# Kernel optimization log

Measured on AMD Instinct MI355X. Metric: run time of the kernel, lower is better.

## Reference

```python
import jax, jax.numpy as jnp
import numpy as np

BATCH_SIZE = 1024
L2_EPS = 1e-12  # tf.nn.l2_normalize epsilon


def setup_inputs() -> dict:
    key = jax.random.key(0)
    k1, k2, k3 = jax.random.split(key, 3)
    worlds = jax.random.normal(k1, (2048, 64), dtype=jnp.float32)   # (n_worlds, d_worlds)
    W = jax.random.normal(k2, (512, 64, 64), dtype=jnp.float32)     # (n_symbols, d, d)
    nullary = jax.random.randint(k3, (1024, 2), 0, 512, dtype=jnp.int32)  # (N, [batch_idx, symbol_idx])
    return {"worlds": worlds, "W": W, "nullary": nullary}


def reference(worlds, W, nullary):
    # Gather per-symbol weight matrices: (N, d, d)
    W_xs = W[nullary[:, 1]]
    # tensordot(W_xs, worlds, axes=[[2],[1]]) -> (N, d, n_worlds)
    x_s = jnp.einsum('nde,we->ndw', W_xs, worlds)
    # L2 normalize over axis=1 (d), matching tf.nn.l2_normalize semantics
    sq = jnp.sum(jnp.square(x_s), axis=1, keepdims=True)
    x_s = x_s * jax.lax.rsqrt(jnp.maximum(sq, L2_EPS))
    # scatter_nd: additive scatter into (batch_size, d, n_worlds)
    d, n_worlds = worlds.shape[1], worlds.shape[0]
    out = jnp.zeros((BATCH_SIZE, d, n_worlds), dtype=x_s.dtype)
    out = out.at[nullary[:, 0]].add(x_s)
    return out
```

## Files before the change

### kernel.cpp

```cpp
#include <hip/hip_runtime.h>

#define NB      1024
#define NWORLD  2048
#define DDIM    64
#define NWMAT   512
#define CONV_BLOCKS 1088
#define LIST_BLOCKS 128
#define GRID_MAIN   6144
#define STASH_ROW   512
#define STASH_ROWS  9
#define FILL_ROW0   (STASH_ROW + STASH_ROWS)
#define FILL_CHUNKS ((NB - FILL_ROW0) * 16)

#define STASH_BYTE  268435456ull
#define OFF_WBF     0ull
#define OFF_WORLDS  4194304ull
#define OFF_DESC    4456448ull

typedef __attribute__((ext_vector_type(4))) float f32x4;
typedef __attribute__((ext_vector_type(8))) short bf16x8;

__device__ __forceinline__ unsigned short f2bf(float f) {
    union { float f; unsigned u; } v; v.f = f;
    unsigned u = v.u;
    u += 0x7fffu + ((u >> 16) & 1u);
    return (unsigned short)(u >> 16);
}

__global__ __launch_bounds__(256)
void prep(const float* __restrict__ W, const float* __restrict__ worlds,
          const int* __restrict__ nullary, char* outb)
{
    unsigned short* Wbf      = (unsigned short*)(outb + STASH_BYTE + OFF_WBF);
    unsigned short* worldsbf = (unsigned short*)(outb + STASH_BYTE + OFF_WORLDS);
    int* descI               = (int*)(outb + STASH_BYTE + OFF_DESC);

    const int bid = blockIdx.x;
    if (bid < CONV_BLOCKS) {
        const int NWE = NWMAT * DDIM * DDIM;
        int i = (bid * 256 + threadIdx.x) * 8;
        const float* src; unsigned short* dst; int off;
        if (i < NWE) { src = W;      dst = Wbf;      off = i; }
        else         { src = worlds; dst = worldsbf; off = i - NWE; }
        f32x4 a = *reinterpret_cast<const f32x4*>(src + off);
        f32x4 b = *reinterpret_cast<const f32x4*>(src + off + 4);
        bf16x8 r;
        r[0] = (short)f2bf(a[0]); r[1] = (short)f2bf(a[1]);
        r[2] = (short)f2bf(a[2]); r[3] = (short)f2bf(a[3]);
        r[4] = (short)f2bf(b[0]); r[5] = (short)f2bf(b[1]);
        r[6] = (short)f2bf(b[2]); r[7] = (short)f2bf(b[3]);
        *reinterpret_cast<bf16x8*>(dst + off) = r;
        return;
    }
    const int r    = (bid - CONV_BLOCKS) * 4 + (threadIdx.x >> 6);
    const int lane = threadIdx.x & 63;
    int base = 0;
    for (int c = 0; c < NB / 64; ++c) {
        const int n = c * 64 + lane;
        const bool m = (nullary[2 * n] == r);
        const unsigned long long mask = __ballot(m);
        if (m) {
            const int pos = base + __popcll(mask & ((1ull << lane) - 1ull));
            if (pos < 31) descI[r * 32 + 1 + pos] = nullary[2 * n + 1];
        }
        base += __popcll(mask);
    }
    if (lane == 0) descI[r * 32] = (base > 31 ? 31 : base);
}

__global__ __launch_bounds__(256)
void main2(char* outb)
{
    const unsigned short* Wbf      = (const unsigned short*)(outb + STASH_BYTE + OFF_WBF);
    const unsigned short* worldsbf = (const unsigned short*)(outb + STASH_BYTE + OFF_WORLDS);
    const int4* desc4              = (const int4*)(outb + STASH_BYTE + OFF_DESC);
    const int*  descI              = (const int*)desc4;
    float* out                     = (float*)outb;

    const int bid = blockIdx.x;
    const int tid = threadIdx.x;
    const f32x4 z = {0.f, 0.f, 0.f, 0.f};

    if (bid % 3 == 2) {
        const int fid = bid / 3;
        for (int chunk = fid; chunk < FILL_CHUNKS; chunk += 2048) {
            const int r = FILL_ROW0 + (chunk >> 4);
            f32x4* o = reinterpret_cast<f32x4*>(out + (size_t)r * DDIM * NWORLD
                                                + (size_t)(chunk & 15) * 8192) + tid;
            #pragma unroll
            for (int j = 0; j < 8; ++j)
                o[j * 256] = z;
        }
        return;
    }

    const int slot = (bid / 3) * 2 + (bid % 3);
    const int r    = slot >> 3;
    const int wtA  = (slot & 7) * 2;

    const int wave = tid >> 6, lane = tid & 63;
    const int col  = lane & 15, krow = lane >> 4;
    const int drow = tid >> 5;
    const int wl   = (tid & 31) * 4;

    bf16x8 bfrag[2][2][2];
    #pragma unroll
    for (int t = 0; t < 2; ++t)
        #pragma unroll
        for (int sub = 0; sub < 2; ++sub) {
            const int w0 = (wtA + t) * 128 + wave * 32 + sub * 16 + col;
            const unsigned short* wp = worldsbf + (size_t)w0 * DDIM + krow * 8;
            bfrag[t][sub][0] = *reinterpret_cast<const bf16x8*>(wp);
            bfrag[t][sub][1] = *reinterpret_cast<const bf16x8*>(wp + 32);
        }

    const int4 h = desc4[r * 8];
    const int cnt = h.x;
    float* orow = out + (size_t)r * DDIM * NWORLD;

    if (cnt == 0) {
        float* obase = orow + wtA * 128;
        #pragma unroll
        for (int k = 0; k < 16; ++k) {
            const int idx = k * 256 + tid;
            const int d  = idx >> 6;
            const int c4 = (idx & 63) * 4;
            *reinterpret_cast<f32x4*>(obase + (size_t)d * NWORLD + c4) = z;
        }
        return;
    }

    __shared__ float T[DDIM][132];

    f32x4 acc[2][2][4];
    #pragma unroll
    for (int t = 0; t < 2; ++t)
        #pragma unroll
        for (int q = 0; q < 2; ++q)
            #pragma unroll
            for (int m = 0; m < 4; ++m)
                acc[t][q][m] = z;

    for (int mi = 0; mi < cnt; ++mi) {
        int b;
        if      (mi == 0) b = h.y;
        else if (mi == 1) b = h.z;
        else if (mi == 2) b = h.w;
        else              b = descI[r * 32 + 1 + mi];
        const unsigned short* Wb = Wbf + (size_t)b * DDIM * DDIM;
        bf16x8 afrag[4][2];
        #pragma unroll
        for (int mt = 0; mt < 4; ++mt) {
            const unsigned short* ap = Wb + (size_t)(mt * 16 + col) * DDIM + krow * 8;
            afrag[mt][0] = *reinterpret_cast<const bf16x8*>(ap);
            afrag[mt][1] = *reinterpret_cast<const bf16x8*>(ap + 32);
        }
        #pragma unroll
        for (int t = 0; t < 2; ++t)
            #pragma unroll
            for (int sub = 0; sub < 2; ++sub) {
                f32x4 x[4];
                #pragma unroll
                for (int mt = 0; mt < 4; ++mt) {
                    f32x4 c = z;
                    c = __builtin_amdgcn_mfma_f32_16x16x32_bf16(afrag[mt][0], bfrag[t][sub][0], c, 0, 0, 0);
                    c = __builtin_amdgcn_mfma_f32_16x16x32_bf16(afrag[mt][1], bfrag[t][sub][1], c, 0, 0, 0);
                    x[mt] = c;
                }
                float p = 0.f;
                #pragma unroll
                for (int mt = 0; mt < 4; ++mt)
                    #pragma unroll
                    for (int j = 0; j < 4; ++j)
                        p += x[mt][j] * x[mt][j];
                p += __shfl_xor(p, 16, 64);
                p += __shfl_xor(p, 32, 64);
                const float s = rsqrtf(fmaxf(p, 1e-12f));
                #pragma unroll
                for (int mt = 0; mt < 4; ++mt)
                    #pragma unroll
                    for (int j = 0; j < 4; ++j)
                        acc[t][sub][mt][j] += x[mt][j] * s;
            }
    }

    #pragma unroll
    for (int t = 0; t < 2; ++t) {
        __syncthreads();
        #pragma unroll
        for (int sub = 0; sub < 2; ++sub)
            #pragma unroll
            for (int mt = 0; mt < 4; ++mt)
                #pragma unroll
                for (int j = 0; j < 4; ++j)
                    T[mt * 16 + krow * 4 + j][wave * 32 + sub * 16 + col] = acc[t][sub][mt][j];
        __syncthreads();

        float* obase = orow + (wtA + t) * 128;
        #pragma unroll
        for (int rd = 0; rd < 8; ++rd) {
            const int d = rd * 8 + drow;
            const f32x4 v = *reinterpret_cast<const f32x4*>(&T[d][wl]);
            *reinterpret_cast<f32x4*>(obase + (size_t)d * NWORLD + wl) = v;
        }
    }
}

__global__ __launch_bounds__(256)
void tail_zero(char* outb)
{
    f32x4* o = reinterpret_cast<f32x4*>(outb + STASH_BYTE);
    const f32x4 z = {0.f, 0.f, 0.f, 0.f};
    const int total = STASH_ROWS * DDIM * NWORLD / 4;
    for (int i = blockIdx.x * 256 + threadIdx.x; i < total; i += 288 * 256)
        o[i] = z;
}

extern "C" void kernel_launch(void* const* d_in, const int* in_sizes, int n_in,
                              void* d_out, int out_size, void* d_ws, size_t ws_size,
                              hipStream_t stream) {
    const float* worlds  = (const float*)d_in[0];
    const float* W       = (const float*)d_in[1];
    const int*   nullary = (const int*)d_in[2];
    char*        outb    = (char*)d_out;

    prep<<<CONV_BLOCKS + LIST_BLOCKS, 256, 0, stream>>>(W, worlds, nullary, outb);
    main2<<<GRID_MAIN, 256, 0, stream>>>(outb);
    tail_zero<<<288, 256, 0, stream>>>(outb);
}
```

Baseline: 118.7 us.

## Swap MFMA operand roles to store output directly without LDS transpose

Makes worlds the A operand and the gathered W matrix the B operand, so each lane's accumulator holds four consecutive world columns for one d row. Results are then written straight to global memory as 16-byte vectors, removing the shared-memory transpose and its barriers. In exchange, the norm reduction now needs four shuffles per element instead of two, and W fragments are reloaded inside the world-tile loop. The global stores are also less coalesced, since each 16-lane group writes a different d row.

```diff
diff --git a/kernel.cpp b/kernel.cpp
--- a/kernel.cpp
+++ b/kernel.cpp
@@ -100,19 +100,15 @@
 
     const int wave = tid >> 6, lane = tid & 63;
     const int col  = lane & 15, krow = lane >> 4;
-    const int drow = tid >> 5;
-    const int wl   = (tid & 31) * 4;
-
-    bf16x8 bfrag[2][2][2];
+    const int wbase = wtA * 128 + wave * 64;
+
+    bf16x8 aw[4][2];
     #pragma unroll
-    for (int t = 0; t < 2; ++t)
-        #pragma unroll
-        for (int sub = 0; sub < 2; ++sub) {
-            const int w0 = (wtA + t) * 128 + wave * 32 + sub * 16 + col;
-            const unsigned short* wp = worldsbf + (size_t)w0 * DDIM + krow * 8;
-            bfrag[t][sub][0] = *reinterpret_cast<const bf16x8*>(wp);
-            bfrag[t][sub][1] = *reinterpret_cast<const bf16x8*>(wp + 32);
-        }
+    for (int mtw = 0; mtw < 4; ++mtw) {
+        const unsigned short* wp = worldsbf + (size_t)(wbase + mtw * 16 + col) * DDIM + krow * 8;
+        aw[mtw][0] = *reinterpret_cast<const bf16x8*>(wp);
+        aw[mtw][1] = *reinterpret_cast<const bf16x8*>(wp + 32);
+    }
 
     const int4 h = desc4[r * 8];
     const int cnt = h.x;
@@ -130,16 +126,12 @@
         return;
     }
 
-    __shared__ float T[DDIM][132];
-
-    f32x4 acc[2][2][4];
+    f32x4 acc[4][4];
     #pragma unroll
-    for (int t = 0; t < 2; ++t)
-        #pragma unroll
-        for (int q = 0; q < 2; ++q)
-            #pragma unroll
-            for (int m = 0; m < 4; ++m)
-                acc[t][q][m] = z;
+    for (int m = 0; m < 4; ++m)
+        #pragma unroll
+        for (int n = 0; n < 4; ++n)
+            acc[m][n] = z;
 
     for (int mi = 0; mi < cnt; ++mi) {
         int b;
@@ -148,62 +140,44 @@
         else if (mi == 2) b = h.w;
         else              b = descI[r * 32 + 1 + mi];
         const unsigned short* Wb = Wbf + (size_t)b * DDIM * DDIM;
-        bf16x8 afrag[4][2];
-        #pragma unroll
-        for (int mt = 0; mt < 4; ++mt) {
-            const unsigned short* ap = Wb + (size_t)(mt * 16 + col) * DDIM + krow * 8;
-            afrag[mt][0] = *reinterpret_cast<const bf16x8*>(ap);
-            afrag[mt][1] = *reinterpret_cast<const bf16x8*>(ap + 32);
-        }
-        #pragma unroll
-        for (int t = 0; t < 2; ++t)
+
+        #pragma unroll
+        for (int mtw = 0; mtw < 4; ++mtw) {
+            f32x4 x[4];
             #pragma unroll
-            for (int sub = 0; sub < 2; ++sub) {
-                f32x4 x[4];
-                #pragma unroll
-                for (int mt = 0; mt < 4; ++mt) {
-                    f32x4 c = z;
-                    c = __builtin_amdgcn_mfma_f32_16x16x32_bf16(afrag[mt][0], bfrag[t][sub][0], c, 0, 0, 0);
-                    c = __builtin_amdgcn_mfma_f32_16x16x32_bf16(afrag[mt][1], bfrag[t][sub][1], c, 0, 0, 0);
-                    x[mt] = c;
-                }
-                float p = 0.f;
-                #pragma unroll
-                for (int mt = 0; mt < 4; ++mt)
-                    #pragma unroll
-                    for (int j = 0; j < 4; ++j)
-                        p += x[mt][j] * x[mt][j];
-                p += __shfl_xor(p, 16, 64);
-                p += __shfl_xor(p, 32, 64);
+            for (int ntd = 0; ntd < 4; ++ntd) {
+                const unsigned short* bp = Wb + (size_t)(ntd * 16 + col) * DDIM + krow * 8;
+                const bf16x8 b0 = *reinterpret_cast<const bf16x8*>(bp);
+                const bf16x8 b1 = *reinterpret_cast<const bf16x8*>(bp + 32);
+                f32x4 c = z;
+                c = __builtin_amdgcn_mfma_f32_16x16x32_bf16(aw[mtw][0], b0, c, 0, 0, 0);
+                c = __builtin_amdgcn_mfma_f32_16x16x32_bf16(aw[mtw][1], b1, c, 0, 0, 0);
+                x[ntd] = c;
+            }
+            #pragma unroll
+            for (int j = 0; j < 4; ++j) {
+                float p = x[0][j] * x[0][j] + x[1][j] * x[1][j]
+                        + x[2][j] * x[2][j] + x[3][j] * x[3][j];
+                p += __shfl_xor(p, 1, 64);
+                p += __shfl_xor(p, 2, 64);
+                p += __shfl_xor(p, 4, 64);
+                p += __shfl_xor(p, 8, 64);
                 const float s = rsqrtf(fmaxf(p, 1e-12f));
                 #pragma unroll
-                for (int mt = 0; mt < 4; ++mt)
-                    #pragma unroll
-                    for (int j = 0; j < 4; ++j)
-                        acc[t][sub][mt][j] += x[mt][j] * s;
+                for (int ntd = 0; ntd < 4; ++ntd)
+                    acc[mtw][ntd][j] += x[ntd][j] * s;
             }
+        }
     }
 
     #pragma unroll
-    for (int t = 0; t < 2; ++t) {
-        __syncthreads();
-        #pragma unroll
-        for (int sub = 0; sub < 2; ++sub)
-            #pragma unroll
-            for (int mt = 0; mt < 4; ++mt)
-                #pragma unroll
-                for (int j = 0; j < 4; ++j)
-                    T[mt * 16 + krow * 4 + j][wave * 32 + sub * 16 + col] = acc[t][sub][mt][j];
-        __syncthreads();
-
-        float* obase = orow + (wtA + t) * 128;
-        #pragma unroll
-        for (int rd = 0; rd < 8; ++rd) {
-            const int d = rd * 8 + drow;
-            const f32x4 v = *reinterpret_cast<const f32x4*>(&T[d][wl]);
-            *reinterpret_cast<f32x4*>(obase + (size_t)d * NWORLD + wl) = v;
-        }
-    }
+    for (int mtw = 0; mtw < 4; ++mtw)
+        #pragma unroll
+        for (int ntd = 0; ntd < 4; ++ntd) {
+            const int d = ntd * 16 + col;
+            float* p = orow + (size_t)d * NWORLD + wbase + mtw * 16 + krow * 4;
+            *reinterpret_cast<f32x4*>(p) = acc[mtw][ntd];
+        }
 }
 
 __global__ __launch_bounds__(256)
```

After: 126.3 us. 1.06x slower.
